# Optimization experiments

Hardware: AMD Instinct MI355X
Metric: run time of the kernel (lower is better)

The kernel has to match this reference:

```python
import jax, jax.numpy as jnp
import numpy as np

N = 50000      # nodes
E = 1600000    # edges (before self loops)
IN = 128       # in_channels
HID = 64       # hidden_channels
HEADS = 2
NEG_SLOPE = 0.2  # PyG GATConv default


def setup_inputs() -> dict:
    key = jax.random.key(0)
    ks = jax.random.split(key, 12)
    s = 0.05
    return {
        "x": jax.random.normal(ks[0], (N, IN), jnp.float32),
        "edge_index": jax.random.randint(ks[1], (2, E), 0, N, dtype=jnp.int32),
        # layer 1: GATConv(IN -> HID, heads=HEADS, concat=True)
        "W1": jax.random.normal(ks[2], (IN, HEADS * HID), jnp.float32) * s,
        "a_src1": jax.random.normal(ks[3], (HEADS, HID), jnp.float32) * s,
        "a_dst1": jax.random.normal(ks[4], (HEADS, HID), jnp.float32) * s,
        "b1": jax.random.normal(ks[5], (HEADS * HID,), jnp.float32) * s,
        # layer 2: GATConv(HEADS*HID -> HID, heads=1, concat=False)
        "W2": jax.random.normal(ks[6], (HEADS * HID, HID), jnp.float32) * s,
        "a_src2": jax.random.normal(ks[7], (1, HID), jnp.float32) * s,
        "a_dst2": jax.random.normal(ks[8], (1, HID), jnp.float32) * s,
        "b2": jax.random.normal(ks[9], (HID,), jnp.float32) * s,
        "lin_w": jax.random.normal(ks[10], (HID, 1), jnp.float32) * s,
        "lin_b": jax.random.normal(ks[11], (1,), jnp.float32) * s,
    }


def gat_layer(x, src, dst, W, a_src, a_dst, b, heads, out_ch, concat, n):
    # linear transform: [n, heads, out_ch]
    h = (x @ W).reshape(n, heads, out_ch)
    # per-node attention logit halves  [n, heads]
    al_src = jnp.sum(h * a_src, axis=-1)
    al_dst = jnp.sum(h * a_dst, axis=-1)
    # per-edge logits (gather) + LeakyReLU  [e, heads]
    e = jax.nn.leaky_relu(al_src[src] + al_dst[dst], negative_slope=NEG_SLOPE)
    # segment softmax over edges grouped by destination node
    m = jax.ops.segment_max(e, dst, num_segments=n)
    ex = jnp.exp(e - m[dst])
    denom = jax.ops.segment_sum(ex, dst, num_segments=n)
    alpha = ex / (denom[dst] + 1e-16)
    # weighted message scatter-add  [n, heads, out_ch]
    out = jax.ops.segment_sum(h[src] * alpha[:, :, None], dst, num_segments=n)
    out = out.reshape(n, heads * out_ch) if concat else out.mean(axis=1)
    return out + b


def reference(x, edge_index, W1, a_src1, a_dst1, b1, W2, a_src2, a_dst2, b2, lin_w, lin_b):
    # PyG GATConv adds self loops by default
    loops = jnp.arange(N, dtype=edge_index.dtype)
    src = jnp.concatenate([edge_index[0], loops])
    dst = jnp.concatenate([edge_index[1], loops])
    h = gat_layer(x, src, dst, W1, a_src1, a_dst1, b1, HEADS, HID, True, N)
    h = jax.nn.elu(h)
    h = gat_layer(h, src, dst, W2, a_src2, a_dst2, b2, 1, HID, False, N)
    return (h @ lin_w + lin_b)[:, 0]  # squeeze(-1) -> [N]
```

## Files before the change

kernel.cpp:

```cpp
#include <hip/hip_runtime.h>
#include <hip/hip_fp16.h>


#define LEAKY(x) ((x) > 0.f ? (x) : 0.2f * (x))

typedef float v2f __attribute__((ext_vector_type(2)));
typedef _Float16 f16x8 __attribute__((ext_vector_type(8)));
typedef __fp16 h16x2 __attribute__((ext_vector_type(2)));
typedef float f32x4 __attribute__((ext_vector_type(4)));


__global__ __launch_bounds__(256) void zero_kernel(int* __restrict__ bcnt,
                                                   int* __restrict__ bcur_rel,
                                                   int* __restrict__ off,
                                                   int B, int n, int Etot) {
  if (threadIdx.x <= (unsigned)B) {
    bcnt[threadIdx.x] = 0;
    bcur_rel[threadIdx.x] = 0;
  }
  if (threadIdx.x == 255) off[n] = Etot;
}


template <int VPT>
__global__ __launch_bounds__(256) void prep_cnt_kernel(const float* __restrict__ W1,
                                                       const float* __restrict__ W2,
                                                       const float* __restrict__ as2,
                                                       const float* __restrict__ ad2,
                                                       const float* __restrict__ lw,
                                                       unsigned short* __restrict__ Wp1,
                                                       float* __restrict__ vsrc2,
                                                       float* __restrict__ vdst2,
                                                       float* __restrict__ vlin,
                                                       const int* __restrict__ ei, int E, int n,
                                                       int* __restrict__ bc, int WB) {
  if ((int)blockIdx.x < WB) {
    int t = blockIdx.x * 256 + threadIdx.x;
    if (t < 16384) {
      int e = t;
      int i = e & 7;
      int c = (e >> 3) & 15;
      int g = (e >> 7) & 3;
      int kk = (e >> 9) & 3;
      int cn = e >> 11;
      int k = kk * 32 + g * 8 + i;
      int col = cn * 16 + c;
      __half h = __float2half(W1[k * 128 + col]);
      Wp1[e] = *(unsigned short*)&h;
    } else if (t < 16384 + 128) {
      int k = t - 16384;
      float a = 0.f, b = 0.f, s = 0.f;
      for (int cc = 0; cc < 64; ++cc) {
        float w = W2[k * 64 + cc];
        a = fmaf(w, as2[cc], a);
        b = fmaf(w, ad2[cc], b);
        s = fmaf(w, lw[cc], s);
      }
      vsrc2[k] = a;
      vdst2[k] = b;
      vlin[k] = s;
    }
    return;
  }
  __shared__ int lc[256];
  int t = threadIdx.x;
  lc[t] = 0;
  __syncthreads();
  int base = (blockIdx.x - WB) * (256 * VPT) + t;
  int tot = E + n;
#pragma unroll
  for (int u = 0; u < VPT; ++u) {
    int i = base + u * 256;
    if (i < tot) {
      int d = (i < E) ? ei[E + i] : (i - E);
      atomicAdd(&lc[d >> 8], 1);
    }
  }
  __syncthreads();
  if (lc[t]) atomicAdd(&bc[t], lc[t]);
}


template <int VPT>
__global__ __launch_bounds__(256) void gemm_scatter_kernel(
    const float* __restrict__ X, const uint4* __restrict__ Wp,
    const float* __restrict__ a_src, const float* __restrict__ a_dst,
    unsigned char* __restrict__ Hout, float2* __restrict__ als, float2* __restrict__ ald,
    const int* __restrict__ ei, int E, int n,
    const int* __restrict__ bcnt, int* __restrict__ bcur_rel,
    unsigned* __restrict__ entries, int B, int GB) {
  if ((int)blockIdx.x < GB) {
    __shared__ float Xl[32 * 132];
    __shared__ float lgt[2][2][2][16];
    int t = threadIdx.x;
    int wave = t >> 6, lane = t & 63;
    int wm = wave >> 1, wn = wave & 1;
    int g = lane >> 4, c = lane & 15;
    int nb0 = blockIdx.x * 32;

    {
      const float4* Xg = (const float4*)X;
      float4* Xs = (float4*)Xl;
#pragma unroll
      for (int u = 0; u < 4; ++u) {
        int idx = u * 256 + t;
        int r = idx >> 5, c4 = idx & 31;
        int row = nb0 + r;
        int rc = row < n ? row : (n - 1);
        Xs[r * 33 + c4] = Xg[(size_t)rc * 32 + c4];
      }
    }
    __syncthreads();

    f16x8 af[4];
    const float* xr = Xl + (wm * 16 + c) * 132 + g * 8;
#pragma unroll
    for (int kk = 0; kk < 4; ++kk) {
      float4 x0 = *(const float4*)(xr + kk * 32);
      float4 x1 = *(const float4*)(xr + kk * 32 + 4);
      union { f16x8 v; h16x2 p[4]; } A;
      A.p[0] = __builtin_amdgcn_cvt_pkrtz(x0.x, x0.y);
      A.p[1] = __builtin_amdgcn_cvt_pkrtz(x0.z, x0.w);
      A.p[2] = __builtin_amdgcn_cvt_pkrtz(x1.x, x1.y);
      A.p[3] = __builtin_amdgcn_cvt_pkrtz(x1.z, x1.w);
      af[kk] = A.v;
    }

    f32x4 acc[4];
    f32x4 z = {0.f, 0.f, 0.f, 0.f};
#pragma unroll
    for (int cn = 0; cn < 4; ++cn) acc[cn] = z;
#pragma unroll
    for (int cn = 0; cn < 4; ++cn) {
      int cng = wn * 4 + cn;
#pragma unroll
      for (int kk = 0; kk < 4; ++kk) {
        union { uint4 u; f16x8 v; } Bf;
        Bf.u = Wp[(cng * 4 + kk) * 64 + lane];
        acc[cn] = __builtin_amdgcn_mfma_f32_16x16x32_f16(af[kk], Bf.v, acc[cn], 0, 0, 0);
      }
    }

    float asv[4], adv[4];
#pragma unroll
    for (int cn = 0; cn < 4; ++cn) {
      int col_l = wn * 64 + cn * 16 + c;
      asv[cn] = a_src[col_l];
      adv[cn] = a_dst[col_l];
    }
    float ps[4] = {0.f, 0.f, 0.f, 0.f};
    float pd[4] = {0.f, 0.f, 0.f, 0.f};
#pragma unroll
    for (int cn = 0; cn < 4; ++cn) {
#pragma unroll
      for (int r = 0; r < 4; ++r) {
        float v = acc[cn][r];
        ps[r] = fmaf(v, asv[cn], ps[r]);
        pd[r] = fmaf(v, adv[cn], pd[r]);
        int noder = nb0 + wm * 16 + g * 4 + r;
        int colg = wn * 64 + cn * 16 + c;
        if (noder < n) {
          int b8 = __builtin_amdgcn_cvt_pk_fp8_f32(v, v, 0, false);
          Hout[(size_t)noder * 128 + colg] = (unsigned char)(b8 & 0xff);
        }
      }
    }
#pragma unroll
    for (int r = 0; r < 4; ++r) {
#pragma unroll
      for (int m = 1; m <= 8; m <<= 1) {
        ps[r] += __shfl_xor(ps[r], m, 64);
        pd[r] += __shfl_xor(pd[r], m, 64);
      }
    }
    if (c == 0) {
#pragma unroll
      for (int r = 0; r < 4; ++r) {
        lgt[wm][wn][0][g * 4 + r] = ps[r];
        lgt[wm][wn][1][g * 4 + r] = pd[r];
      }
    }
    __syncthreads();
    if (t < 32) {
      int wmm = t >> 4, row = t & 15;
      int node = nb0 + wmm * 16 + row;
      if (node < n) {
        als[node] = make_float2(lgt[wmm][0][0][row], lgt[wmm][1][0][row]);
        ald[node] = make_float2(lgt[wmm][0][1][row], lgt[wmm][1][1][row]);
      }
    }
    return;
  }
  __shared__ int lc[256];
  __shared__ int lbase[256];
  __shared__ int bscan[256];
  int t = threadIdx.x;
  lc[t] = 0;
  int v = (t < B) ? bcnt[t] : 0;
  bscan[t] = v;
  __syncthreads();
  for (int s = 1; s < 256; s <<= 1) {
    int a = (t >= s) ? bscan[t - s] : 0;
    __syncthreads();
    bscan[t] += a;
    __syncthreads();
  }
  int excl = bscan[t] - v;

  int base = (blockIdx.x - GB) * (256 * VPT) + t;
  int tot = E + n;
  int bb[VPT], ll[VPT];
  unsigned pk[VPT];
#pragma unroll
  for (int u = 0; u < VPT; ++u) {
    int i = base + u * 256;
    bb[u] = -1;
    if (i < tot) {
      int s, d;
      if (i < E) { s = ei[i]; d = ei[E + i]; }
      else       { s = d = i - E; }
      int b = d >> 8;
      bb[u] = b;
      ll[u] = atomicAdd(&lc[b], 1);
      pk[u] = (unsigned)s | ((unsigned)(d & 255) << 16);
    }
  }
  __syncthreads();
  if (lc[t]) lbase[t] = excl + atomicAdd(&bcur_rel[t], lc[t]);
  __syncthreads();
#pragma unroll
  for (int u = 0; u < VPT; ++u)
    if (bb[u] >= 0) entries[lbase[bb[u]] + ll[u]] = pk[u];
}


__global__ __launch_bounds__(1024) void csr_build_kernel(const unsigned* __restrict__ entries,
                                                         const int* __restrict__ bcnt,
                                                         int* __restrict__ off,
                                                         unsigned short* __restrict__ eps,
                                                         int n, int B) {
  __shared__ int bscan[256];
  __shared__ int hist[256];
  __shared__ int scn[256];
  __shared__ int cur[256];
  int b = blockIdx.x, t = threadIdx.x;
  if (t < 256) bscan[t] = (t < B) ? bcnt[t] : 0;
  __syncthreads();
  for (int s = 1; s < 256; s <<= 1) {
    int a = (t >= (unsigned)s && t < 256) ? bscan[t - s] : 0;
    __syncthreads();
    if (t < 256) bscan[t] += a;
    __syncthreads();
  }
  int k0 = (b == 0) ? 0 : bscan[b - 1];
  int k1 = bscan[b];

  if (t < 256) hist[t] = 0;
  __syncthreads();
  for (int k = k0 + t; k < k1; k += 1024) atomicAdd(&hist[(entries[k] >> 16) & 255], 1);
  __syncthreads();
  int hv = (t < 256) ? hist[t] : 0;
  if (t < 256) scn[t] = hv;
  __syncthreads();
  for (int s = 1; s < 256; s <<= 1) {
    int a = (t >= (unsigned)s && t < 256) ? scn[t - s] : 0;
    __syncthreads();
    if (t < 256) scn[t] += a;
    __syncthreads();
  }
  if (t < 256) {
    int excl = scn[t] - hv;
    int d = (b << 8) + t;
    if (d < n) off[d] = k0 + excl;
    cur[t] = k0 + excl;
  }
  __syncthreads();
  for (int k = k0 + t; k < k1; k += 1024) {
    unsigned e = entries[k];
    unsigned dl = (e >> 16) & 255;
    int p = atomicAdd(&cur[dl], 1);
    eps[p] = (unsigned short)(e & 0xffffu);
  }
}


__global__ __launch_bounds__(256) void agg1_kernel(const unsigned char* __restrict__ Hb8,
                                                   const float2* __restrict__ als,
                                                   const float2* __restrict__ ald,
                                                   const unsigned short* __restrict__ eps,
                                                   const int* __restrict__ off,
                                                   const float* __restrict__ b1,
                                                   const float* __restrict__ vsrc2,
                                                   const float* __restrict__ vdst2,
                                                   const float* __restrict__ vlin,
                                                   float2* __restrict__ gsrc,
                                                   float* __restrict__ adst2, int n) {
  __shared__ float wlds[4][128];
  int wid = (blockIdx.x * 256 + threadIdx.x) >> 6;
  int lane = threadIdx.x & 63;
  if (wid >= n) return;
  wid = __builtin_amdgcn_readfirstlane(wid);
  int wslot = (threadIdx.x >> 6) & 3;
  int half = lane >> 5;
  int k0 = off[wid], k1 = off[wid + 1];
  const unsigned short* Hu = (const unsigned short*)Hb8;
  float2 advv = ald[wid];
  float* wrow = &wlds[wslot][half << 6];

  float ax = 0.f, ay = 0.f, den0 = 0.f, den1 = 0.f;

  for (int kb = k0; kb < k1; kb += 64) {
    int rem = min(k1 - kb, 64);
    int e = kb + (lane < rem ? lane : rem - 1);
    unsigned pp = eps[e];
    float2 l = als[pp];
    float g0 = __expf(LEAKY(l.x + advv.x));
    float g1 = __expf(LEAKY(l.y + advv.y));
    wlds[wslot][lane] = g0;
    wlds[wslot][64 + lane] = g1;
    if (rem == 64) {
      den0 += g0;
      den1 += g1;
    } else if (lane < rem) {
      den0 += g0;
      den1 += g1;
    }

#define EDGE1(jj)                                                                   \
  {                                                                                 \
    unsigned p = (unsigned)__builtin_amdgcn_readlane((int)pp, (jj));                \
    float w = wrow[(jj)];                                                           \
    unsigned short hv = Hu[(p << 6) | (unsigned)lane];                              \
    v2f hf = __builtin_amdgcn_cvt_pk_f32_fp8((int)hv, false);                       \
    ax = fmaf(hf.x, w, ax);                                                         \
    ay = fmaf(hf.y, w, ay);                                                         \
  }

    int nb = rem >> 3;
    for (int b = 0; b < nb; ++b) {
      int jb = b << 3;
#pragma unroll
      for (int j = 0; j < 8; ++j) EDGE1(jb + j);
    }
    for (int jj = nb << 3; jj < rem; ++jj) EDGE1(jj);
#undef EDGE1
  }

#pragma unroll
  for (int m = 1; m <= 32; m <<= 1) {
    den0 += __shfl_xor(den0, m, 64);
    den1 += __shfl_xor(den1, m, 64);
  }
  float den = half ? den1 : den0;

  float inv = 1.f / (den + 1e-16f);
  float2 bv = ((const float2*)b1)[lane];
  float r0 = ax * inv + bv.x;
  float r1 = ay * inv + bv.y;
  r0 = r0 > 0.f ? r0 : (__expf(r0) - 1.f);
  r1 = r1 > 0.f ? r1 : (__expf(r1) - 1.f);
  float2 vs = ((const float2*)vsrc2)[lane];
  float2 vd = ((const float2*)vdst2)[lane];
  float2 vl = ((const float2*)vlin)[lane];
  float ps = r0 * vs.x + r1 * vs.y;
  float pd = r0 * vd.x + r1 * vd.y;
  float sv = r0 * vl.x + r1 * vl.y;
#pragma unroll
  for (int m = 1; m <= 32; m <<= 1) {
    ps += __shfl_xor(ps, m, 64);
    pd += __shfl_xor(pd, m, 64);
    sv += __shfl_xor(sv, m, 64);
  }
  if (lane == 0) {
    gsrc[wid] = make_float2(ps, sv);
    adst2[wid] = pd;
  }
}


__global__ __launch_bounds__(256) void agg2_kernel(const float2* __restrict__ gsrc,
                                                   const float* __restrict__ adst2,
                                                   const unsigned short* __restrict__ eps,
                                                   const int* __restrict__ off,
                                                   const float* __restrict__ b2,
                                                   const float* __restrict__ lin_w,
                                                   const float* __restrict__ lin_b,
                                                   float* __restrict__ out, int n) {
  int wid = (blockIdx.x * 256 + threadIdx.x) >> 6;
  int lane = threadIdx.x & 63;
  if (wid >= n) return;
  wid = __builtin_amdgcn_readfirstlane(wid);
  int k0 = off[wid], k1 = off[wid + 1];
  float adv = adst2[wid];

  float num = 0.f, den = 0.f;
  for (int kb = k0; kb < k1; kb += 64) {
    int e = kb + lane;
    bool ok = e < k1;
    unsigned pp = eps[ok ? e : k0];
    float2 g = gsrc[pp];
    float w = ok ? __expf(LEAKY(g.x + adv)) : 0.f;
    num = fmaf(w, g.y, num);
    den += w;
  }
  float bt = b2[lane] * lin_w[lane];
#pragma unroll
  for (int m = 1; m <= 32; m <<= 1) {
    num += __shfl_xor(num, m, 64);
    den += __shfl_xor(den, m, 64);
    bt  += __shfl_xor(bt, m, 64);
  }
  if (lane == 0) out[wid] = num / (den + 1e-16f) + bt + lin_b[0];
}


static inline size_t alignup(size_t v) { return (v + 255) & ~(size_t)255; }

extern "C" void kernel_launch(void* const* d_in, const int* in_sizes, int n_in,
                              void* d_out, int out_size, void* d_ws, size_t ws_size,
                              hipStream_t stream) {
  const float* x   = (const float*)d_in[0];
  const int*   ei  = (const int*)d_in[1];
  const float* W1  = (const float*)d_in[2];
  const float* as1 = (const float*)d_in[3];
  const float* ad1 = (const float*)d_in[4];
  const float* b1  = (const float*)d_in[5];
  const float* W2  = (const float*)d_in[6];
  const float* as2 = (const float*)d_in[7];
  const float* ad2 = (const float*)d_in[8];
  const float* b2  = (const float*)d_in[9];
  const float* lw  = (const float*)d_in[10];
  const float* lb  = (const float*)d_in[11];
  float* out = (float*)d_out;

  const int N = out_size;
  const int E = in_sizes[1] / 2;
  const int Etot = E + N;
  const int B = (N + 255) >> 8;

  char* p = (char*)d_ws;
  int* bcnt = (int*)p;  p += alignup((size_t)(B + 1) * 4);
  int* bcur_rel = (int*)p; p += alignup((size_t)(B + 1) * 4);
  unsigned* entries = (unsigned*)p; p += alignup((size_t)Etot * 4);
  int* off  = (int*)p;  p += alignup((size_t)(N + 1) * 4);
  unsigned short* eps = (unsigned short*)p; p += alignup((size_t)Etot * 2);
  float2* als = (float2*)p; p += alignup((size_t)N * 8);
  float2* ald = (float2*)p; p += alignup((size_t)N * 8);
  float2* gsrc = (float2*)p; p += alignup((size_t)N * 8);
  float* adst2 = (float*)p; p += alignup((size_t)N * 4);
  unsigned char* h1b = (unsigned char*)p; p += alignup((size_t)N * 128);
  unsigned short* wp1 = (unsigned short*)p; p += alignup((size_t)16384 * 2);
  float* vsrc2 = (float*)p; p += alignup((size_t)128 * 4);
  float* vdst2 = (float*)p; p += alignup((size_t)128 * 4);
  float* vlin  = (float*)p; p += alignup((size_t)128 * 4);

  constexpr int VPT = 8;
  int egrid = (Etot + 256 * VPT - 1) / (256 * VPT);
  constexpr int WB = 65;
  int GB = (N + 31) / 32;

  zero_kernel<<<1, 256, 0, stream>>>(bcnt, bcur_rel, off, B, N, Etot);
  prep_cnt_kernel<VPT><<<WB + egrid, 256, 0, stream>>>(
      W1, W2, as2, ad2, lw, wp1, vsrc2, vdst2, vlin, ei, E, N, bcnt, WB);
  gemm_scatter_kernel<VPT><<<GB + egrid, 256, 0, stream>>>(
      x, (const uint4*)wp1, as1, ad1, h1b, als, ald,
      ei, E, N, bcnt, bcur_rel, entries, B, GB);
  csr_build_kernel<<<B, 1024, 0, stream>>>(entries, bcnt, off, eps, N, B);

  agg1_kernel<<<(N + 3) / 4, 256, 0, stream>>>(h1b, als, ald, eps, off, b1,
                                               vsrc2, vdst2, vlin, gsrc, adst2, N);
  agg2_kernel<<<(N + 3) / 4, 256, 0, stream>>>(gsrc, adst2, eps, off, b2, lw, lb, out, N);
}
```

Measured before the change: 130.6 us.

## Process two edges per iteration in agg1 with 4-byte fp8 loads per lane

Measured after the change: 127.6 us. -2.3%, faster.

```diff
diff --git a/kernel.cpp b/kernel.cpp
--- a/kernel.cpp
+++ b/kernel.cpp
@@ -301,13 +301,15 @@
   if (wid >= n) return;
   wid = __builtin_amdgcn_readfirstlane(wid);
   int wslot = (threadIdx.x >> 6) & 3;
-  int half = lane >> 5;
+  int sel = lane >> 5;
+  int c31 = lane & 31;
+  int head = c31 >> 4;
   int k0 = off[wid], k1 = off[wid + 1];
-  const unsigned short* Hu = (const unsigned short*)Hb8;
+  const unsigned* Hd = (const unsigned*)Hb8;
   float2 advv = ald[wid];
-  float* wrow = &wlds[wslot][half << 6];
-
-  float ax = 0.f, ay = 0.f, den0 = 0.f, den1 = 0.f;
+  int wbase = head * 64 + sel;
+
+  float a0 = 0.f, a1 = 0.f, a2 = 0.f, a3 = 0.f, den0 = 0.f, den1 = 0.f;
 
   for (int kb = k0; kb < k1; kb += 64) {
     int rem = min(k1 - kb, 64);
@@ -316,57 +318,64 @@
     float2 l = als[pp];
     float g0 = __expf(LEAKY(l.x + advv.x));
     float g1 = __expf(LEAKY(l.y + advv.y));
-    wlds[wslot][lane] = g0;
-    wlds[wslot][64 + lane] = g1;
-    if (rem == 64) {
-      den0 += g0;
-      den1 += g1;
-    } else if (lane < rem) {
-      den0 += g0;
-      den1 += g1;
-    }
-
-#define EDGE1(jj)                                                                   \
+    bool ok = lane < rem;
+    wlds[wslot][lane] = ok ? g0 : 0.f;
+    wlds[wslot][64 + lane] = ok ? g1 : 0.f;
+    if (ok) { den0 += g0; den1 += g1; }
+    int npair = (rem + 1) >> 1;
+
+#define PAIR1(qq)                                                                   \
   {                                                                                 \
-    unsigned p = (unsigned)__builtin_amdgcn_readlane((int)pp, (jj));                \
-    float w = wrow[(jj)];                                                           \
-    unsigned short hv = Hu[(p << 6) | (unsigned)lane];                              \
-    v2f hf = __builtin_amdgcn_cvt_pk_f32_fp8((int)hv, false);                       \
-    ax = fmaf(hf.x, w, ax);                                                         \
-    ay = fmaf(hf.y, w, ay);                                                         \
-  }
-
-    int nb = rem >> 3;
+    unsigned p = (unsigned)__shfl((int)pp, ((qq) << 1) + sel, 64);                  \
+    float w = wlds[wslot][wbase + ((qq) << 1)];                                     \
+    unsigned hv = Hd[p * 32u + (unsigned)c31];                                      \
+    v2f lo = __builtin_amdgcn_cvt_pk_f32_fp8((int)hv, false);                       \
+    v2f hi = __builtin_amdgcn_cvt_pk_f32_fp8((int)hv, true);                        \
+    a0 = fmaf(lo.x, w, a0);                                                         \
+    a1 = fmaf(lo.y, w, a1);                                                         \
+    a2 = fmaf(hi.x, w, a2);                                                         \
+    a3 = fmaf(hi.y, w, a3);                                                         \
+  }
+
+    int nb = npair >> 3;
     for (int b = 0; b < nb; ++b) {
-      int jb = b << 3;
-#pragma unroll
-      for (int j = 0; j < 8; ++j) EDGE1(jb + j);
-    }
-    for (int jj = nb << 3; jj < rem; ++jj) EDGE1(jj);
-#undef EDGE1
-  }
-
+      int qb = b << 3;
+#pragma unroll
+      for (int q = 0; q < 8; ++q) PAIR1(qb + q);
+    }
+    for (int q = nb << 3; q < npair; ++q) PAIR1(q);
+#undef PAIR1
+  }
+
+  a0 += __shfl_xor(a0, 32, 64);
+  a1 += __shfl_xor(a1, 32, 64);
+  a2 += __shfl_xor(a2, 32, 64);
+  a3 += __shfl_xor(a3, 32, 64);
 #pragma unroll
   for (int m = 1; m <= 32; m <<= 1) {
     den0 += __shfl_xor(den0, m, 64);
     den1 += __shfl_xor(den1, m, 64);
   }
-  float den = half ? den1 : den0;
+  float den = head ? den1 : den0;
 
   float inv = 1.f / (den + 1e-16f);
-  float2 bv = ((const float2*)b1)[lane];
-  float r0 = ax * inv + bv.x;
-  float r1 = ay * inv + bv.y;
+  float4 bv = ((const float4*)b1)[c31];
+  float r0 = a0 * inv + bv.x;
+  float r1 = a1 * inv + bv.y;
+  float r2 = a2 * inv + bv.z;
+  float r3 = a3 * inv + bv.w;
   r0 = r0 > 0.f ? r0 : (__expf(r0) - 1.f);
   r1 = r1 > 0.f ? r1 : (__expf(r1) - 1.f);
-  float2 vs = ((const float2*)vsrc2)[lane];
-  float2 vd = ((const float2*)vdst2)[lane];
-  float2 vl = ((const float2*)vlin)[lane];
-  float ps = r0 * vs.x + r1 * vs.y;
-  float pd = r0 * vd.x + r1 * vd.y;
-  float sv = r0 * vl.x + r1 * vl.y;
-#pragma unroll
-  for (int m = 1; m <= 32; m <<= 1) {
+  r2 = r2 > 0.f ? r2 : (__expf(r2) - 1.f);
+  r3 = r3 > 0.f ? r3 : (__expf(r3) - 1.f);
+  float4 vs = ((const float4*)vsrc2)[c31];
+  float4 vd = ((const float4*)vdst2)[c31];
+  float4 vl = ((const float4*)vlin)[c31];
+  float ps = r0 * vs.x + r1 * vs.y + r2 * vs.z + r3 * vs.w;
+  float pd = r0 * vd.x + r1 * vd.y + r2 * vd.z + r3 * vd.w;
+  float sv = r0 * vl.x + r1 * vl.y + r2 * vl.z + r3 * vl.w;
+#pragma unroll
+  for (int m = 1; m <= 16; m <<= 1) {
     ps += __shfl_xor(ps, m, 64);
     pd += __shfl_xor(pd, m, 64);
     sv += __shfl_xor(sv, m, 64);
```
